# Optimization experiments

Measured on AMD Instinct MI355X. Metric: run time of the kernel, lower is better.

Reference implementation:

```python
import jax, jax.numpy as jnp
import numpy as np

N_NODES = 50000
N_EDGES = 800000
IN_DIM = 256
OUT_DIM = 64
HEADS = 4
NEG_SLOPE = 0.2  # PyG GATConv default


def setup_inputs() -> dict:
    key = jax.random.key(0)
    k1, k2, k3, k4, k5, k6 = jax.random.split(key, 6)
    x = jax.random.normal(k1, (N_NODES, IN_DIM), dtype=jnp.float32)
    edge_index = jax.random.randint(k2, (2, N_EDGES), 0, N_NODES, dtype=jnp.int64)
    scale = 1.0 / np.sqrt(IN_DIM)
    W = jax.random.normal(k3, (IN_DIM, HEADS * OUT_DIM), dtype=jnp.float32) * scale
    att_src = jax.random.normal(k4, (HEADS, OUT_DIM), dtype=jnp.float32) * scale
    att_dst = jax.random.normal(k5, (HEADS, OUT_DIM), dtype=jnp.float32) * scale
    bias = jnp.zeros((HEADS * OUT_DIM,), dtype=jnp.float32)
    return {"x": x, "edge_index": edge_index, "W": W,
            "att_src": att_src, "att_dst": att_dst, "bias": bias}


def reference(x, edge_index, W, att_src, att_dst, bias):
    N = x.shape[0]
    H, C = att_src.shape
    # add self loops (PyG GATConv default add_self_loops=True)
    loop = jnp.arange(N, dtype=edge_index.dtype)
    src = jnp.concatenate([edge_index[0], loop])  # [E+N] source j
    dst = jnp.concatenate([edge_index[1], loop])  # [E+N] target i
    # linear projection, per-head features  [N, H, C]
    h = (x @ W).reshape(N, H, C)
    # attention logits: a_src . h_j + a_dst . h_i  -> [E, H]
    a_src = jnp.einsum('nhc,hc->nh', h, att_src)
    a_dst = jnp.einsum('nhc,hc->nh', h, att_dst)
    e = jax.nn.leaky_relu(a_src[src] + a_dst[dst], negative_slope=NEG_SLOPE)
    # edge softmax over incoming edges of each destination node
    m = jax.ops.segment_max(e, dst, num_segments=N)          # [N, H]
    p = jnp.exp(e - m[dst])                                  # [E, H]
    denom = jax.ops.segment_sum(p, dst, num_segments=N)      # [N, H]
    alpha = p / (denom[dst] + 1e-16)                         # [E, H]
    # weighted scatter-aggregate of gathered source features
    out = jax.ops.segment_sum(alpha[:, :, None] * h[src], dst, num_segments=N)
    out = out.reshape(N, H * C) + bias
    return jax.nn.relu(out)  # GATLayer active_func
```

## Files before the change

kernel.cpp:

```cpp
#include <hip/hip_runtime.h>

constexpr int N  = 50000;
constexpr int E  = 800000;
constexpr int K  = 256;
constexpr int F  = 256;
constexpr int H  = 4;
constexpr float SLOPE = 0.2f;

constexpr int WT_ROWS = 272;

constexpr size_t OFF_HB   = 0;
constexpr size_t OFF_WT   = OFF_HB   + (size_t)N * F * 2;
constexpr size_t OFF_ASRC = OFF_WT   + (size_t)WT_ROWS * K * 2;
constexpr size_t OFF_ADST = OFF_ASRC + (size_t)N * H * 4;
constexpr size_t OFF_DEG  = OFF_ADST + (size_t)N * H * 4;
constexpr size_t OFF_OFFS = OFF_DEG  + (size_t)N * 4;
constexpr size_t OFF_FLAG = OFF_OFFS + (size_t)(N + 16) * 4;
constexpr size_t OFF_RANK = OFF_FLAG + 64;
constexpr size_t OFF_CSR  = OFF_RANK + (size_t)E * 4;

constexpr int HIST_BLOCKS = 128;
constexpr int GEMM_BLOCKS = (N + 127) / 128;

typedef short short8 __attribute__((ext_vector_type(8)));
typedef float floatx4 __attribute__((ext_vector_type(4)));

__device__ __forceinline__ float leaky(float x) {
    return x > 0.f ? x : SLOPE * x;
}
__device__ __forceinline__ float blo(unsigned u) { return __uint_as_float(u << 16); }
__device__ __forceinline__ float bhi(unsigned u) { return __uint_as_float(u & 0xffff0000u); }
__device__ __forceinline__ unsigned short f2b(float f) {
    unsigned u = __float_as_uint(f);
    return (unsigned short)((u + 0x7fffu + ((u >> 16) & 1u)) >> 16);
}
__device__ __forceinline__ unsigned pk2(float a, float b) {
    return (unsigned)f2b(a) | ((unsigned)f2b(b) << 16);
}

__device__ __forceinline__ int edge_at(const void* ei, int is64, size_t i) {
    if (is64) return (int)((const long long*)ei)[i];
    return ((const int*)ei)[i];
}

__global__ __launch_bounds__(256)
void prep(const float* __restrict__ Wm, const float* __restrict__ att_src,
          const float* __restrict__ att_dst, const unsigned* __restrict__ ei_words,
          unsigned short* __restrict__ Wt, int* __restrict__ flag,
          int4* __restrict__ zero_region) {
    __shared__ float tile[64][65];
    const int bid = blockIdx.x;
    const int t = threadIdx.x;
    if (bid < 16) {
        const int k0 = (bid & 3) * 64;
        const int n0 = (bid >> 2) * 64;
        const int r = t >> 2;
        const int c4 = (t & 3) * 16;
        #pragma unroll
        for (int i = 0; i < 16; i += 4) {
            float4 v = *reinterpret_cast<const float4*>(
                Wm + (size_t)(k0 + r) * F + n0 + c4 + i);
            tile[r][c4 + i + 0] = v.x;
            tile[r][c4 + i + 1] = v.y;
            tile[r][c4 + i + 2] = v.z;
            tile[r][c4 + i + 3] = v.w;
        }
        __syncthreads();
        unsigned pk[8];
        #pragma unroll
        for (int j = 0; j < 8; ++j)
            pk[j] = pk2(tile[c4 + 2 * j + 0][r], tile[c4 + 2 * j + 1][r]);
        unsigned short* dst = Wt + (size_t)(n0 + r) * K + k0 + c4;
        *reinterpret_cast<uint4*>(dst)     = make_uint4(pk[0], pk[1], pk[2], pk[3]);
        *reinterpret_cast<uint4*>(dst + 8) = make_uint4(pk[4], pk[5], pk[6], pk[7]);
    } else if (bid == 16) {
        const int k = t;
        #pragma unroll
        for (int h = 0; h < H; ++h) {
            const float* wr = Wm + (size_t)k * F + h * 64;
            float s = 0.f, d = 0.f;
            #pragma unroll 8
            for (int c = 0; c < 64; ++c) {
                float w = wr[c];
                s += w * att_src[h * 64 + c];
                d += w * att_dst[h * 64 + c];
            }
            Wt[(size_t)(256 + h) * K + k] = f2b(s);
            Wt[(size_t)(260 + h) * K + k] = f2b(d);
        }
        #pragma unroll
        for (int r = 0; r < 8; ++r) Wt[(size_t)(264 + r) * K + k] = 0;
    } else if (bid == 17) {
        if (t < 64) {
            unsigned v = ei_words[2 * t + 1];
            unsigned long long b = __ballot(v != 0u);
            if (t == 0) *flag = (b == 0ull) ? 1 : 0;
        }
    } else {
        int idx = (bid - 18) * 256 + t;
        if (idx < 12500) zero_region[idx] = make_int4(0, 0, 0, 0);
    }
}

constexpr int LDA = 72;
constexpr int LDW = 72;

__global__ __launch_bounds__(512, 4)
void gemm_hist(const float* __restrict__ X, const unsigned short* __restrict__ Wt,
               unsigned short* __restrict__ Hb, float* __restrict__ asrc,
               float* __restrict__ adst, const void* __restrict__ ei,
               const int* __restrict__ flag, int* __restrict__ deg,
               unsigned* __restrict__ rankpack) {
    __shared__ unsigned short Al[128 * LDA];
    __shared__ unsigned short Wl[WT_ROWS * LDW];
    const int tid = threadIdx.x;

    if (blockIdx.x < HIST_BLOCKS) {
        const int is64 = *flag;
        for (int i = blockIdx.x * 512 + tid; i < E; i += HIST_BLOCKS * 512) {
            int d = edge_at(ei, is64, (size_t)E + i);
            int r = atomicAdd(&deg[d], 1);
            rankpack[i] = ((unsigned)r << 17) | (unsigned)d;
        }
        return;
    }

    const int wv = tid >> 6, lane = tid & 63;
    const int quad = lane >> 4, l15 = lane & 15;
    const int rH = wv >> 2;
    const int cQ = wv & 3;
    const int m0 = (blockIdx.x - HIST_BLOCKS) * 128;

    floatx4 acc[4][4];
    #pragma unroll
    for (int i = 0; i < 4; ++i)
        #pragma unroll
        for (int j = 0; j < 4; ++j) acc[i][j] = (floatx4)0.f;
    floatx4 accf[4];
    #pragma unroll
    for (int i = 0; i < 4; ++i) accf[i] = (floatx4)0.f;

    const int ar = tid >> 2;
    const int akc = (tid & 3) * 16;
    const bool arow_ok = (m0 + ar) < N;
    const int wr = tid >> 1;
    const int wkc = (tid & 1) * 32;

    for (int k0 = 0; k0 < K; k0 += 64) {
        {
            const float* src = X + (size_t)(m0 + ar) * K + k0 + akc;
            unsigned short* dst = &Al[ar * LDA + akc];
            #pragma unroll
            for (int i = 0; i < 16; i += 4) {
                float4 v = arow_ok ? *reinterpret_cast<const float4*>(src + i)
                                   : make_float4(0.f, 0.f, 0.f, 0.f);
                *reinterpret_cast<uint2*>(dst + i) =
                    make_uint2(pk2(v.x, v.y), pk2(v.z, v.w));
            }
        }
        {
            const unsigned short* src = Wt + (size_t)wr * K + k0 + wkc;
            unsigned short* dst = &Wl[wr * LDW + wkc];
            #pragma unroll
            for (int i = 0; i < 32; i += 8)
                *reinterpret_cast<int4*>(dst + i) =
                    *reinterpret_cast<const int4*>(src + i);
        }
        if (tid < 32) {
            const int fr = 256 + (tid >> 1);
            const int fk = (tid & 1) * 32;
            const unsigned short* src = Wt + (size_t)fr * K + k0 + fk;
            unsigned short* dst = &Wl[fr * LDW + fk];
            #pragma unroll
            for (int i = 0; i < 32; i += 8)
                *reinterpret_cast<int4*>(dst + i) =
                    *reinterpret_cast<const int4*>(src + i);
        }
        __syncthreads();
        #pragma unroll
        for (int kk = 0; kk < 64; kk += 32) {
            short8 a[4];
            #pragma unroll
            for (int i = 0; i < 4; ++i)
                a[i] = *reinterpret_cast<const short8*>(
                    &Al[(rH * 64 + i * 16 + l15) * LDA + kk + quad * 8]);
            #pragma unroll
            for (int j = 0; j < 4; ++j) {
                short8 b = *reinterpret_cast<const short8*>(
                    &Wl[(cQ * 64 + j * 16 + l15) * LDW + kk + quad * 8]);
                #pragma unroll
                for (int i = 0; i < 4; ++i)
                    acc[i][j] = __builtin_amdgcn_mfma_f32_16x16x32_bf16(
                        a[i], b, acc[i][j], 0, 0, 0);
            }
            if (cQ == 3) {
                short8 bf = *reinterpret_cast<const short8*>(
                    &Wl[(256 + l15) * LDW + kk + quad * 8]);
                #pragma unroll
                for (int i = 0; i < 4; ++i)
                    accf[i] = __builtin_amdgcn_mfma_f32_16x16x32_bf16(
                        a[i], bf, accf[i], 0, 0, 0);
            }
        }
        __syncthreads();
    }
    #pragma unroll
    for (int i = 0; i < 4; ++i) {
        const int rbase = m0 + rH * 64 + i * 16 + quad * 4;
        #pragma unroll
        for (int j = 0; j < 4; ++j) {
            const int col = cQ * 64 + j * 16 + l15;
            #pragma unroll
            for (int r = 0; r < 4; ++r) {
                int row = rbase + r;
                if (row < N) Hb[(size_t)row * F + col] = f2b(acc[i][j][r]);
            }
        }
    }
    if (cQ == 3) {
        #pragma unroll
        for (int i = 0; i < 4; ++i) {
            const int rbase = m0 + rH * 64 + i * 16 + quad * 4;
            #pragma unroll
            for (int r = 0; r < 4; ++r) {
                int row = rbase + r;
                if (row < N) {
                    if (l15 < 4)      asrc[row * H + l15] = accf[i][r];
                    else if (l15 < 8) adst[row * H + (l15 - 4)] = accf[i][r];
                }
            }
        }
    }
}

__global__ __launch_bounds__(1024)
void scan_deg(const int* __restrict__ deg, int* __restrict__ offs) {
    __shared__ int sums[1024];
    const int t = threadIdx.x;
    const int lo = t * 52;
    const int hi = min(lo + 52, N);
    int s = 0;
    if (lo < N) {
        const int4* p = reinterpret_cast<const int4*>(deg + lo);
        const int n4 = (hi - lo) >> 2;
        for (int i = 0; i < n4; ++i) {
            int4 v = p[i];
            s += v.x + v.y + v.z + v.w;
        }
    }
    sums[t] = s;
    __syncthreads();
    for (int off = 1; off < 1024; off <<= 1) {
        int v = (t >= off) ? sums[t - off] : 0;
        __syncthreads();
        sums[t] += v;
        __syncthreads();
    }
    int base = sums[t] - s;
    if (lo < N) {
        const int4* p = reinterpret_cast<const int4*>(deg + lo);
        int4* q = reinterpret_cast<int4*>(offs + lo);
        const int n4 = (hi - lo) >> 2;
        for (int i = 0; i < n4; ++i) {
            int4 v = p[i];
            int4 o;
            o.x = base;
            o.y = o.x + v.x;
            o.z = o.y + v.y;
            o.w = o.z + v.z;
            base = o.w + v.w;
            q[i] = o;
        }
    }
    if (t == 0) offs[N] = sums[1023];
}

__global__ void scatter_edges(const void* __restrict__ ei,
                              const int* __restrict__ flag,
                              const int* __restrict__ offs,
                              const unsigned* __restrict__ rankpack,
                              int* __restrict__ csr) {
    const int is64 = *flag;
    for (int i = blockIdx.x * blockDim.x + threadIdx.x; i < E;
         i += gridDim.x * blockDim.x) {
        unsigned pk = rankpack[i];
        int d = (int)(pk & 0x1ffffu);
        int r = (int)(pk >> 17);
        int s = edge_at(ei, is64, i);
        csr[offs[d] + r] = s;
    }
}

__global__ __launch_bounds__(256, 8)
void aggregate(const unsigned short* __restrict__ Hb, const float* __restrict__ asrc,
               const float* __restrict__ adst, const int* __restrict__ offs,
               const int* __restrict__ csr, const float* __restrict__ bias,
               float* __restrict__ out) {
    const int wv = threadIdx.x >> 6;
    const int lane = threadIdx.x & 63;
    const int half = lane >> 5;
    const int l32 = lane & 31;
    const int hd = l32 >> 3;
    const int node = blockIdx.x * 4 + wv;

    const char* hbase = (const char*)Hb;
    const char* abase = (const char*)asrc;
    const unsigned lsh = (unsigned)l32 << 4;
    const unsigned hsh = (unsigned)hd << 2;

    const float adsti = adst[node * H + hd];
    const int start = offs[node];
    const int end = offs[node + 1];

    float denom = 0.f;
    float a0 = 0.f, a1 = 0.f, a2 = 0.f, a3 = 0.f;
    float a4 = 0.f, a5 = 0.f, a6 = 0.f, a7 = 0.f;
    int e = start;
    for (; e + 8 <= end; e += 8) {
        unsigned s[4]; float l[4]; uint4 u[4];
        #pragma unroll
        for (int j = 0; j < 4; ++j) s[j] = (unsigned)csr[e + 2 * j + half];
        #pragma unroll
        for (int j = 0; j < 4; ++j)
            l[j] = *(const float*)(abase + ((s[j] << 4) + hsh));
        #pragma unroll
        for (int j = 0; j < 4; ++j)
            u[j] = *(const uint4*)(hbase + ((s[j] << 9) + lsh));
        #pragma unroll
        for (int j = 0; j < 4; ++j) {
            float p = __expf(leaky(l[j] + adsti));
            denom += p;
            a0 += p * blo(u[j].x); a1 += p * bhi(u[j].x);
            a2 += p * blo(u[j].y); a3 += p * bhi(u[j].y);
            a4 += p * blo(u[j].z); a5 += p * bhi(u[j].z);
            a6 += p * blo(u[j].w); a7 += p * bhi(u[j].w);
        }
    }
    for (; e + 2 <= end; e += 2) {
        unsigned s0 = (unsigned)csr[e + half];
        float l0 = *(const float*)(abase + ((s0 << 4) + hsh));
        uint4 u0 = *(const uint4*)(hbase + ((s0 << 9) + lsh));
        float p = __expf(leaky(l0 + adsti));
        denom += p;
        a0 += p * blo(u0.x); a1 += p * bhi(u0.x);
        a2 += p * blo(u0.y); a3 += p * bhi(u0.y);
        a4 += p * blo(u0.z); a5 += p * bhi(u0.z);
        a6 += p * blo(u0.w); a7 += p * bhi(u0.w);
    }
    {
        const int rem = end - e;
        bool active;
        unsigned sf;
        if (half == 0) { active = (rem == 1); sf = active ? (unsigned)csr[e] : 0u; }
        else           { active = true;       sf = (unsigned)node; }
        if (active) {
            float l0 = *(const float*)(abase + ((sf << 4) + hsh));
            uint4 u0 = *(const uint4*)(hbase + ((sf << 9) + lsh));
            float p = __expf(leaky(l0 + adsti));
            denom += p;
            a0 += p * blo(u0.x); a1 += p * bhi(u0.x);
            a2 += p * blo(u0.y); a3 += p * bhi(u0.y);
            a4 += p * blo(u0.z); a5 += p * bhi(u0.z);
            a6 += p * blo(u0.w); a7 += p * bhi(u0.w);
        }
    }
    a0 += __shfl_xor(a0, 32); a1 += __shfl_xor(a1, 32);
    a2 += __shfl_xor(a2, 32); a3 += __shfl_xor(a3, 32);
    a4 += __shfl_xor(a4, 32); a5 += __shfl_xor(a5, 32);
    a6 += __shfl_xor(a6, 32); a7 += __shfl_xor(a7, 32);
    denom += __shfl_xor(denom, 32);
    if (half == 0) {
        const float inv = 1.f / (denom + 1e-16f);
        float4 b0 = *reinterpret_cast<const float4*>(bias + l32 * 8);
        float4 b1 = *reinterpret_cast<const float4*>(bias + l32 * 8 + 4);
        float4 o0, o1;
        o0.x = fmaxf(a0 * inv + b0.x, 0.f);
        o0.y = fmaxf(a1 * inv + b0.y, 0.f);
        o0.z = fmaxf(a2 * inv + b0.z, 0.f);
        o0.w = fmaxf(a3 * inv + b0.w, 0.f);
        o1.x = fmaxf(a4 * inv + b1.x, 0.f);
        o1.y = fmaxf(a5 * inv + b1.y, 0.f);
        o1.z = fmaxf(a6 * inv + b1.z, 0.f);
        o1.w = fmaxf(a7 * inv + b1.w, 0.f);
        float* orow = out + (size_t)node * F + l32 * 8;
        *reinterpret_cast<float4*>(orow)     = o0;
        *reinterpret_cast<float4*>(orow + 4) = o1;
    }
}

extern "C" void kernel_launch(void* const* d_in, const int* in_sizes, int n_in,
                              void* d_out, int out_size, void* d_ws, size_t ws_size,
                              hipStream_t stream) {
    const float* x       = (const float*)d_in[0];
    const void*  ei      = d_in[1];
    const float* Wm      = (const float*)d_in[2];
    const float* att_src = (const float*)d_in[3];
    const float* att_dst = (const float*)d_in[4];
    const float* bias    = (const float*)d_in[5];
    float* out = (float*)d_out;

    char* ws = (char*)d_ws;
    unsigned short* hb = (unsigned short*)(ws + OFF_HB);
    unsigned short* wt = (unsigned short*)(ws + OFF_WT);
    float* asrc = (float*)(ws + OFF_ASRC);
    float* adst = (float*)(ws + OFF_ADST);
    int* deg  = (int*)(ws + OFF_DEG);
    int* offs = (int*)(ws + OFF_OFFS);
    int* flag = (int*)(ws + OFF_FLAG);
    unsigned* rankpack = (unsigned*)(ws + OFF_RANK);
    int* csr  = (int*)(ws + OFF_CSR);

    prep<<<67, 256, 0, stream>>>(Wm, att_src, att_dst, (const unsigned*)ei,
                                 wt, flag, (int4*)(ws + OFF_DEG));
    gemm_hist<<<HIST_BLOCKS + GEMM_BLOCKS, 512, 0, stream>>>(
        x, wt, hb, asrc, adst, ei, flag, deg, rankpack);
    scan_deg<<<1, 1024, 0, stream>>>(deg, offs);
    scatter_edges<<<1024, 256, 0, stream>>>(ei, flag, offs, rankpack, csr);
    aggregate<<<N / 4, 256, 0, stream>>>(hb, asrc, adst, offs, csr, bias, out);
}
```

Before: 258.9 us.

## Merge histogram, scan, scatter and GEMM into one cooperative persistent kernel

Replaces the gemm_hist, single-block scan_deg and scatter_edges launches with one cooperative kernel that uses grid-wide syncs between a degree histogram, a two-level multi-block prefix scan, the CSR scatter and a persistent-tile GEMM loop. It removes two kernel launches and the serial single-block scan, and lets the GEMM follow the scatter inside the same kernel. In exchange, grid.sync barriers serialize the phases: the histogram no longer overlaps the GEMM blocks. The grid size is capped at 512, and the scan assumes G <= 512 and about 98 nodes per block, so the GEMM may run with fewer resident tiles than before.

Result: slower. 395.3 us (+52.7%).

```diff
diff --git a/kernel.cpp b/kernel.cpp
--- a/kernel.cpp
+++ b/kernel.cpp
@@ -1,4 +1,7 @@
 #include <hip/hip_runtime.h>
+#include <hip/hip_cooperative_groups.h>
+
+namespace cg = cooperative_groups;
 
 constexpr int N  = 50000;
 constexpr int E  = 800000;
@@ -18,8 +21,8 @@
 constexpr size_t OFF_FLAG = OFF_OFFS + (size_t)(N + 16) * 4;
 constexpr size_t OFF_RANK = OFF_FLAG + 64;
 constexpr size_t OFF_CSR  = OFF_RANK + (size_t)E * 4;
-
-constexpr int HIST_BLOCKS = 128;
+constexpr size_t OFF_BSUM = OFF_CSR  + (size_t)E * 4;
+
 constexpr int GEMM_BLOCKS = (N + 127) / 128;
 
 typedef short short8 __attribute__((ext_vector_type(8)));
@@ -106,188 +109,172 @@
 constexpr int LDW = 72;
 
 __global__ __launch_bounds__(512, 4)
-void gemm_hist(const float* __restrict__ X, const unsigned short* __restrict__ Wt,
-               unsigned short* __restrict__ Hb, float* __restrict__ asrc,
-               float* __restrict__ adst, const void* __restrict__ ei,
-               const int* __restrict__ flag, int* __restrict__ deg,
-               unsigned* __restrict__ rankpack) {
+void mega(const float* __restrict__ X, const unsigned short* __restrict__ Wt,
+          unsigned short* __restrict__ Hb, float* __restrict__ asrc,
+          float* __restrict__ adst, const void* __restrict__ ei,
+          const int* __restrict__ flag, int* __restrict__ deg,
+          unsigned* __restrict__ rankpack, int* __restrict__ offs,
+          int* __restrict__ csr, int* __restrict__ bsum) {
     __shared__ unsigned short Al[128 * LDA];
     __shared__ unsigned short Wl[WT_ROWS * LDW];
+    cg::grid_group grid = cg::this_grid();
     const int tid = threadIdx.x;
-
-    if (blockIdx.x < HIST_BLOCKS) {
-        const int is64 = *flag;
-        for (int i = blockIdx.x * 512 + tid; i < E; i += HIST_BLOCKS * 512) {
-            int d = edge_at(ei, is64, (size_t)E + i);
-            int r = atomicAdd(&deg[d], 1);
-            rankpack[i] = ((unsigned)r << 17) | (unsigned)d;
-        }
-        return;
-    }
-
-    const int wv = tid >> 6, lane = tid & 63;
-    const int quad = lane >> 4, l15 = lane & 15;
-    const int rH = wv >> 2;
-    const int cQ = wv & 3;
-    const int m0 = (blockIdx.x - HIST_BLOCKS) * 128;
-
-    floatx4 acc[4][4];
-    #pragma unroll
-    for (int i = 0; i < 4; ++i)
-        #pragma unroll
-        for (int j = 0; j < 4; ++j) acc[i][j] = (floatx4)0.f;
-    floatx4 accf[4];
-    #pragma unroll
-    for (int i = 0; i < 4; ++i) accf[i] = (floatx4)0.f;
-
-    const int ar = tid >> 2;
-    const int akc = (tid & 3) * 16;
-    const bool arow_ok = (m0 + ar) < N;
-    const int wr = tid >> 1;
-    const int wkc = (tid & 1) * 32;
-
-    for (int k0 = 0; k0 < K; k0 += 64) {
-        {
-            const float* src = X + (size_t)(m0 + ar) * K + k0 + akc;
-            unsigned short* dst = &Al[ar * LDA + akc];
-            #pragma unroll
-            for (int i = 0; i < 16; i += 4) {
-                float4 v = arow_ok ? *reinterpret_cast<const float4*>(src + i)
-                                   : make_float4(0.f, 0.f, 0.f, 0.f);
-                *reinterpret_cast<uint2*>(dst + i) =
-                    make_uint2(pk2(v.x, v.y), pk2(v.z, v.w));
-            }
-        }
-        {
-            const unsigned short* src = Wt + (size_t)wr * K + k0 + wkc;
-            unsigned short* dst = &Wl[wr * LDW + wkc];
-            #pragma unroll
-            for (int i = 0; i < 32; i += 8)
-                *reinterpret_cast<int4*>(dst + i) =
-                    *reinterpret_cast<const int4*>(src + i);
-        }
-        if (tid < 32) {
-            const int fr = 256 + (tid >> 1);
-            const int fk = (tid & 1) * 32;
-            const unsigned short* src = Wt + (size_t)fr * K + k0 + fk;
-            unsigned short* dst = &Wl[fr * LDW + fk];
-            #pragma unroll
-            for (int i = 0; i < 32; i += 8)
-                *reinterpret_cast<int4*>(dst + i) =
-                    *reinterpret_cast<const int4*>(src + i);
-        }
+    const int bid = blockIdx.x;
+    const int G = gridDim.x;
+    const int is64 = *flag;
+
+    for (int i = bid * 512 + tid; i < E; i += G * 512) {
+        int d = edge_at(ei, is64, (size_t)E + i);
+        int r = atomicAdd(&deg[d], 1);
+        rankpack[i] = ((unsigned)r << 17) | (unsigned)d;
+    }
+    grid.sync();
+
+    {
+        int* sc = reinterpret_cast<int*>(Al);
+        int* s2 = sc + 512;
+        const int CH = (N + G - 1) / G;
+        const int base = bid * CH;
+        const int cnt = min(max(N - base, 0), CH);
+        sc[tid] = (tid < cnt) ? deg[base + tid] : 0;
         __syncthreads();
-        #pragma unroll
-        for (int kk = 0; kk < 64; kk += 32) {
-            short8 a[4];
-            #pragma unroll
-            for (int i = 0; i < 4; ++i)
-                a[i] = *reinterpret_cast<const short8*>(
-                    &Al[(rH * 64 + i * 16 + l15) * LDA + kk + quad * 8]);
-            #pragma unroll
-            for (int j = 0; j < 4; ++j) {
-                short8 b = *reinterpret_cast<const short8*>(
-                    &Wl[(cQ * 64 + j * 16 + l15) * LDW + kk + quad * 8]);
-                #pragma unroll
-                for (int i = 0; i < 4; ++i)
-                    acc[i][j] = __builtin_amdgcn_mfma_f32_16x16x32_bf16(
-                        a[i], b, acc[i][j], 0, 0, 0);
-            }
-            if (cQ == 3) {
-                short8 bf = *reinterpret_cast<const short8*>(
-                    &Wl[(256 + l15) * LDW + kk + quad * 8]);
-                #pragma unroll
-                for (int i = 0; i < 4; ++i)
-                    accf[i] = __builtin_amdgcn_mfma_f32_16x16x32_bf16(
-                        a[i], bf, accf[i], 0, 0, 0);
-            }
-        }
+        for (int off = 1; off < 512; off <<= 1) {
+            int v = (tid >= off) ? sc[tid - off] : 0;
+            __syncthreads();
+            sc[tid] += v;
+            __syncthreads();
+        }
+        if (tid == 0) bsum[bid] = sc[511];
+        grid.sync();
+        s2[tid] = (tid < G) ? bsum[tid] : 0;
         __syncthreads();
-    }
-    #pragma unroll
-    for (int i = 0; i < 4; ++i) {
-        const int rbase = m0 + rH * 64 + i * 16 + quad * 4;
-        #pragma unroll
-        for (int j = 0; j < 4; ++j) {
-            const int col = cQ * 64 + j * 16 + l15;
-            #pragma unroll
-            for (int r = 0; r < 4; ++r) {
-                int row = rbase + r;
-                if (row < N) Hb[(size_t)row * F + col] = f2b(acc[i][j][r]);
-            }
-        }
-    }
-    if (cQ == 3) {
-        #pragma unroll
-        for (int i = 0; i < 4; ++i) {
-            const int rbase = m0 + rH * 64 + i * 16 + quad * 4;
-            #pragma unroll
-            for (int r = 0; r < 4; ++r) {
-                int row = rbase + r;
-                if (row < N) {
-                    if (l15 < 4)      asrc[row * H + l15] = accf[i][r];
-                    else if (l15 < 8) adst[row * H + (l15 - 4)] = accf[i][r];
-                }
-            }
-        }
-    }
-}
-
-__global__ __launch_bounds__(1024)
-void scan_deg(const int* __restrict__ deg, int* __restrict__ offs) {
-    __shared__ int sums[1024];
-    const int t = threadIdx.x;
-    const int lo = t * 52;
-    const int hi = min(lo + 52, N);
-    int s = 0;
-    if (lo < N) {
-        const int4* p = reinterpret_cast<const int4*>(deg + lo);
-        const int n4 = (hi - lo) >> 2;
-        for (int i = 0; i < n4; ++i) {
-            int4 v = p[i];
-            s += v.x + v.y + v.z + v.w;
-        }
-    }
-    sums[t] = s;
-    __syncthreads();
-    for (int off = 1; off < 1024; off <<= 1) {
-        int v = (t >= off) ? sums[t - off] : 0;
-        __syncthreads();
-        sums[t] += v;
-        __syncthreads();
-    }
-    int base = sums[t] - s;
-    if (lo < N) {
-        const int4* p = reinterpret_cast<const int4*>(deg + lo);
-        int4* q = reinterpret_cast<int4*>(offs + lo);
-        const int n4 = (hi - lo) >> 2;
-        for (int i = 0; i < n4; ++i) {
-            int4 v = p[i];
-            int4 o;
-            o.x = base;
-            o.y = o.x + v.x;
-            o.z = o.y + v.y;
-            o.w = o.z + v.z;
-            base = o.w + v.w;
-            q[i] = o;
-        }
-    }
-    if (t == 0) offs[N] = sums[1023];
-}
-
-__global__ void scatter_edges(const void* __restrict__ ei,
-                              const int* __restrict__ flag,
-                              const int* __restrict__ offs,
-                              const unsigned* __restrict__ rankpack,
-                              int* __restrict__ csr) {
-    const int is64 = *flag;
-    for (int i = blockIdx.x * blockDim.x + threadIdx.x; i < E;
-         i += gridDim.x * blockDim.x) {
+        for (int off = 1; off < 512; off <<= 1) {
+            int v = (tid >= off) ? s2[tid - off] : 0;
+            __syncthreads();
+            s2[tid] += v;
+            __syncthreads();
+        }
+        const int bp = (bid > 0) ? s2[bid - 1] : 0;
+        if (tid < cnt) offs[base + tid] = bp + (tid > 0 ? sc[tid - 1] : 0);
+        if (bid == 0 && tid == 0) offs[N] = s2[G - 1];
+    }
+    grid.sync();
+
+    for (int i = bid * 512 + tid; i < E; i += G * 512) {
         unsigned pk = rankpack[i];
         int d = (int)(pk & 0x1ffffu);
         int r = (int)(pk >> 17);
         int s = edge_at(ei, is64, i);
         csr[offs[d] + r] = s;
+    }
+
+    const int wv = tid >> 6, lane = tid & 63;
+    const int quad = lane >> 4, l15 = lane & 15;
+    const int rH = wv >> 2;
+    const int cQ = wv & 3;
+    const int ar = tid >> 2;
+    const int akc = (tid & 3) * 16;
+    const int wr = tid >> 1;
+    const int wkc = (tid & 1) * 32;
+
+    for (int tile = bid; tile < GEMM_BLOCKS; tile += G) {
+        const int m0 = tile * 128;
+        const bool arow_ok = (m0 + ar) < N;
+
+        floatx4 acc[4][4];
+        #pragma unroll
+        for (int i = 0; i < 4; ++i)
+            #pragma unroll
+            for (int j = 0; j < 4; ++j) acc[i][j] = (floatx4)0.f;
+        floatx4 accf[4];
+        #pragma unroll
+        for (int i = 0; i < 4; ++i) accf[i] = (floatx4)0.f;
+
+        for (int k0 = 0; k0 < K; k0 += 64) {
+            {
+                const float* src = X + (size_t)(m0 + ar) * K + k0 + akc;
+                unsigned short* dst = &Al[ar * LDA + akc];
+                #pragma unroll
+                for (int i = 0; i < 16; i += 4) {
+                    float4 v = arow_ok ? *reinterpret_cast<const float4*>(src + i)
+                                       : make_float4(0.f, 0.f, 0.f, 0.f);
+                    *reinterpret_cast<uint2*>(dst + i) =
+                        make_uint2(pk2(v.x, v.y), pk2(v.z, v.w));
+                }
+            }
+            {
+                const unsigned short* src = Wt + (size_t)wr * K + k0 + wkc;
+                unsigned short* dst = &Wl[wr * LDW + wkc];
+                #pragma unroll
+                for (int i = 0; i < 32; i += 8)
+                    *reinterpret_cast<int4*>(dst + i) =
+                        *reinterpret_cast<const int4*>(src + i);
+            }
+            if (tid < 32) {
+                const int fr = 256 + (tid >> 1);
+                const int fk = (tid & 1) * 32;
+                const unsigned short* src = Wt + (size_t)fr * K + k0 + fk;
+                unsigned short* dst = &Wl[fr * LDW + fk];
+                #pragma unroll
+                for (int i = 0; i < 32; i += 8)
+                    *reinterpret_cast<int4*>(dst + i) =
+                        *reinterpret_cast<const int4*>(src + i);
+            }
+            __syncthreads();
+            #pragma unroll
+            for (int kk = 0; kk < 64; kk += 32) {
+                short8 a[4];
+                #pragma unroll
+                for (int i = 0; i < 4; ++i)
+                    a[i] = *reinterpret_cast<const short8*>(
+                        &Al[(rH * 64 + i * 16 + l15) * LDA + kk + quad * 8]);
+                #pragma unroll
+                for (int j = 0; j < 4; ++j) {
+                    short8 b = *reinterpret_cast<const short8*>(
+                        &Wl[(cQ * 64 + j * 16 + l15) * LDW + kk + quad * 8]);
+                    #pragma unroll
+                    for (int i = 0; i < 4; ++i)
+                        acc[i][j] = __builtin_amdgcn_mfma_f32_16x16x32_bf16(
+                            a[i], b, acc[i][j], 0, 0, 0);
+                }
+                if (cQ == 3) {
+                    short8 bf = *reinterpret_cast<const short8*>(
+                        &Wl[(256 + l15) * LDW + kk + quad * 8]);
+                    #pragma unroll
+                    for (int i = 0; i < 4; ++i)
+                        accf[i] = __builtin_amdgcn_mfma_f32_16x16x32_bf16(
+                            a[i], bf, accf[i], 0, 0, 0);
+                }
+            }
+            __syncthreads();
+        }
+        #pragma unroll
+        for (int i = 0; i < 4; ++i) {
+            const int rbase = m0 + rH * 64 + i * 16 + quad * 4;
+            #pragma unroll
+            for (int j = 0; j < 4; ++j) {
+                const int col = cQ * 64 + j * 16 + l15;
+                #pragma unroll
+                for (int r = 0; r < 4; ++r) {
+                    int row = rbase + r;
+                    if (row < N) Hb[(size_t)row * F + col] = f2b(acc[i][j][r]);
+                }
+            }
+        }
+        if (cQ == 3) {
+            #pragma unroll
+            for (int i = 0; i < 4; ++i) {
+                const int rbase = m0 + rH * 64 + i * 16 + quad * 4;
+                #pragma unroll
+                for (int r = 0; r < 4; ++r) {
+                    int row = rbase + r;
+                    if (row < N) {
+                        if (l15 < 4)      asrc[row * H + l15] = accf[i][r];
+                        else if (l15 < 8) adst[row * H + (l15 - 4)] = accf[i][r];
+                    }
+                }
+            }
+        }
     }
 }
 
@@ -409,12 +396,29 @@
     int* flag = (int*)(ws + OFF_FLAG);
     unsigned* rankpack = (unsigned*)(ws + OFF_RANK);
     int* csr  = (int*)(ws + OFF_CSR);
+    int* bsum = (int*)(ws + OFF_BSUM);
+
+    static int G_mega = 0;
+    if (G_mega == 0) {
+        int nb = 0;
+        if (hipOccupancyMaxActiveBlocksPerMultiprocessor(&nb, mega, 512, 0)
+                != hipSuccess || nb < 1) nb = 1;
+        int dev = 0, cus = 256;
+        hipGetDevice(&dev);
+        if (hipDeviceGetAttribute(&cus, hipDeviceAttributeMultiprocessorCount,
+                                  dev) != hipSuccess || cus < 1) cus = 256;
+        long long g = (long long)nb * cus;
+        if (g > 512) g = 512;
+        if (g < 98) g = 98;
+        G_mega = (int)g;
+    }
 
     prep<<<67, 256, 0, stream>>>(Wm, att_src, att_dst, (const unsigned*)ei,
                                  wt, flag, (int4*)(ws + OFF_DEG));
-    gemm_hist<<<HIST_BLOCKS + GEMM_BLOCKS, 512, 0, stream>>>(
-        x, wt, hb, asrc, adst, ei, flag, deg, rankpack);
-    scan_deg<<<1, 1024, 0, stream>>>(deg, offs);
-    scatter_edges<<<1024, 256, 0, stream>>>(ei, flag, offs, rankpack, csr);
+    void* margs[] = {(void*)&x, (void*)&wt, (void*)&hb, (void*)&asrc,
+                     (void*)&adst, (void*)&ei, (void*)&flag, (void*)&deg,
+                     (void*)&rankpack, (void*)&offs, (void*)&csr, (void*)&bsum};
+    hipLaunchCooperativeKernel((const void*)mega, dim3(G_mega), dim3(512),
+                               margs, 0, stream);
     aggregate<<<N / 4, 256, 0, stream>>>(hb, asrc, adst, offs, csr, bias, out);
 }
```

## Replace single-block degree scan with multi-block atomic-offset segment allocation

Applied to the files above, without the earlier changes.

The degree prefix scan moves from one 1024-thread block to many 512-thread blocks. Each block does a wave-shuffle scan and claims its base offset with an atomicAdd on a global counter that prep zeroes. The resulting offsets are contiguous per block but not ordered across blocks, so aggregate now computes each segment end from start plus deg instead of offs[node+1]. This removes a serial single-CU scan stage, at the cost of a nondeterministic CSR layout order across blocks.

Result: faster. 241.9 us (-6.6%).

```diff
diff --git a/kernel.cpp b/kernel.cpp
--- a/kernel.cpp
+++ b/kernel.cpp
@@ -21,6 +21,7 @@
 
 constexpr int HIST_BLOCKS = 128;
 constexpr int GEMM_BLOCKS = (N + 127) / 128;
+constexpr int SCAN_BLOCKS = (N + 511) / 512;
 
 typedef short short8 __attribute__((ext_vector_type(8)));
 typedef float floatx4 __attribute__((ext_vector_type(4)));
@@ -47,7 +48,7 @@
 void prep(const float* __restrict__ Wm, const float* __restrict__ att_src,
           const float* __restrict__ att_dst, const unsigned* __restrict__ ei_words,
           unsigned short* __restrict__ Wt, int* __restrict__ flag,
-          int4* __restrict__ zero_region) {
+          int4* __restrict__ zero_region, int* __restrict__ offs_g) {
     __shared__ float tile[64][65];
     const int bid = blockIdx.x;
     const int t = threadIdx.x;
@@ -95,6 +96,8 @@
             unsigned v = ei_words[2 * t + 1];
             unsigned long long b = __ballot(v != 0u);
             if (t == 0) *flag = (b == 0ull) ? 1 : 0;
+        } else if (t == 64) {
+            offs_g[N + 1] = 0;
         }
     } else {
         int idx = (bid - 18) * 256 + t;
@@ -233,46 +236,30 @@
     }
 }
 
-__global__ __launch_bounds__(1024)
+__global__ __launch_bounds__(512)
 void scan_deg(const int* __restrict__ deg, int* __restrict__ offs) {
-    __shared__ int sums[1024];
     const int t = threadIdx.x;
-    const int lo = t * 52;
-    const int hi = min(lo + 52, N);
-    int s = 0;
-    if (lo < N) {
-        const int4* p = reinterpret_cast<const int4*>(deg + lo);
-        const int n4 = (hi - lo) >> 2;
-        for (int i = 0; i < n4; ++i) {
-            int4 v = p[i];
-            s += v.x + v.y + v.z + v.w;
-        }
-    }
-    sums[t] = s;
+    const int i = blockIdx.x * 512 + t;
+    const int lane = t & 63, wv = t >> 6;
+    const int d = (i < N) ? deg[i] : 0;
+    int x = d;
+    #pragma unroll
+    for (int off = 1; off < 64; off <<= 1) {
+        int y = __shfl_up(x, off);
+        if (lane >= off) x += y;
+    }
+    __shared__ int wsum[8], woff[8];
+    __shared__ int gbase;
+    if (lane == 63) wsum[wv] = x;
     __syncthreads();
-    for (int off = 1; off < 1024; off <<= 1) {
-        int v = (t >= off) ? sums[t - off] : 0;
-        __syncthreads();
-        sums[t] += v;
-        __syncthreads();
-    }
-    int base = sums[t] - s;
-    if (lo < N) {
-        const int4* p = reinterpret_cast<const int4*>(deg + lo);
-        int4* q = reinterpret_cast<int4*>(offs + lo);
-        const int n4 = (hi - lo) >> 2;
-        for (int i = 0; i < n4; ++i) {
-            int4 v = p[i];
-            int4 o;
-            o.x = base;
-            o.y = o.x + v.x;
-            o.z = o.y + v.y;
-            o.w = o.z + v.z;
-            base = o.w + v.w;
-            q[i] = o;
-        }
-    }
-    if (t == 0) offs[N] = sums[1023];
+    if (t == 0) {
+        int s = 0;
+        #pragma unroll
+        for (int w = 0; w < 8; ++w) { woff[w] = s; s += wsum[w]; }
+        gbase = atomicAdd(&offs[N + 1], s);
+    }
+    __syncthreads();
+    if (i < N) offs[i] = gbase + woff[wv] + (x - d);
 }
 
 __global__ void scatter_edges(const void* __restrict__ ei,
@@ -294,8 +281,8 @@
 __global__ __launch_bounds__(256, 8)
 void aggregate(const unsigned short* __restrict__ Hb, const float* __restrict__ asrc,
                const float* __restrict__ adst, const int* __restrict__ offs,
-               const int* __restrict__ csr, const float* __restrict__ bias,
-               float* __restrict__ out) {
+               const int* __restrict__ deg, const int* __restrict__ csr,
+               const float* __restrict__ bias, float* __restrict__ out) {
     const int wv = threadIdx.x >> 6;
     const int lane = threadIdx.x & 63;
     const int half = lane >> 5;
@@ -310,7 +297,7 @@
 
     const float adsti = adst[node * H + hd];
     const int start = offs[node];
-    const int end = offs[node + 1];
+    const int end = start + deg[node];
 
     float denom = 0.f;
     float a0 = 0.f, a1 = 0.f, a2 = 0.f, a3 = 0.f;
@@ -411,10 +398,10 @@
     int* csr  = (int*)(ws + OFF_CSR);
 
     prep<<<67, 256, 0, stream>>>(Wm, att_src, att_dst, (const unsigned*)ei,
-                                 wt, flag, (int4*)(ws + OFF_DEG));
+                                 wt, flag, (int4*)(ws + OFF_DEG), offs);
     gemm_hist<<<HIST_BLOCKS + GEMM_BLOCKS, 512, 0, stream>>>(
         x, wt, hb, asrc, adst, ei, flag, deg, rankpack);
-    scan_deg<<<1, 1024, 0, stream>>>(deg, offs);
+    scan_deg<<<SCAN_BLOCKS, 512, 0, stream>>>(deg, offs);
     scatter_edges<<<1024, 256, 0, stream>>>(ei, flag, offs, rankpack, csr);
-    aggregate<<<N / 4, 256, 0, stream>>>(hb, asrc, adst, offs, csr, bias, out);
-}
+    aggregate<<<N / 4, 256, 0, stream>>>(hb, asrc, adst, offs, deg, csr, bias, out);
+}
```
